# Optimization experiments

Hardware: AMD Instinct MI355X
Metric: run time of the kernel (lower is better)

The kernel has to match this reference:

```python
import jax, jax.numpy as jnp
import numpy as np
from jax import lax

# Model dims (mamba_ssm defaults: d_state=16, d_conv=4, expand=2, dt_rank=ceil(d_model/16))
V = 16384       # vocab_size
D = 1024        # embedding_dim / d_model
C_CLS = 128     # num_CLS_classes
D_INNER = 2 * D # expand * d_model = 2048
N = 16          # d_state
K = 4           # d_conv
DT_RANK = (D + 15) // 16  # 64
B, L = 4, 512


def setup_inputs() -> dict:
    key = jax.random.key(0)
    ks = jax.random.split(key, 12)
    s = 0.02
    tokens = jax.random.randint(ks[0], (B, L), 0, V, dtype=jnp.int64)
    embedding = jax.random.normal(ks[1], (V, D), jnp.float32) * s
    in_proj_w = jax.random.normal(ks[2], (2 * D_INNER, D), jnp.float32) * s
    conv_w = jax.random.normal(ks[3], (D_INNER, 1, K), jnp.float32) * 0.1
    conv_b = jnp.zeros((D_INNER,), jnp.float32)
    x_proj_w = jax.random.normal(ks[4], (DT_RANK + 2 * N, D_INNER), jnp.float32) * s
    dt_proj_w = jax.random.normal(ks[5], (D_INNER, DT_RANK), jnp.float32) * s
    dt_proj_b = jax.random.uniform(ks[6], (D_INNER,), jnp.float32, -4.0, -2.0)  # softplus -> small dt
    A_log = jnp.log(jnp.broadcast_to(jnp.arange(1, N + 1, dtype=jnp.float32), (D_INNER, N)))
    D_param = jnp.ones((D_INNER,), jnp.float32)
    out_proj_w = jax.random.normal(ks[7], (D, D_INNER), jnp.float32) * s
    recon_w = jax.random.normal(ks[8], (V, D), jnp.float32) * s
    cls_w = jax.random.normal(ks[9], (C_CLS, D), jnp.float32) * s
    return dict(tokens=tokens, embedding=embedding, in_proj_w=in_proj_w,
                conv_w=conv_w, conv_b=conv_b, x_proj_w=x_proj_w,
                dt_proj_w=dt_proj_w, dt_proj_b=dt_proj_b, A_log=A_log,
                D_param=D_param, out_proj_w=out_proj_w, recon_w=recon_w, cls_w=cls_w)


def _mamba(h, in_proj_w, conv_w, conv_b, x_proj_w, dt_proj_w, dt_proj_b, A_log, D_param, out_proj_w):
    # h: (B, L, D)
    xz = jnp.einsum('bld,ed->ble', h, in_proj_w)          # (B, L, 2*D_INNER)
    x, z = jnp.split(xz, 2, axis=-1)                      # each (B, L, D_INNER)
    # causal depthwise conv1d along L
    xt = jnp.swapaxes(x, 1, 2)                            # (B, D_INNER, L)
    xt = lax.conv_general_dilated(xt, conv_w, window_strides=(1,),
                                  padding=[(K - 1, 0)],
                                  feature_group_count=D_INNER,
                                  dimension_numbers=('NCH', 'OIH', 'NCH'))
    xt = xt + conv_b[None, :, None]
    x = jax.nn.silu(jnp.swapaxes(xt, 1, 2))               # (B, L, D_INNER)
    # input-dependent dt, B, C
    x_dbl = jnp.einsum('bld,ed->ble', x, x_proj_w)        # (B, L, DT_RANK+2N)
    dt, Bm, Cm = jnp.split(x_dbl, [DT_RANK, DT_RANK + N], axis=-1)
    delta = jax.nn.softplus(jnp.einsum('blr,dr->bld', dt, dt_proj_w) + dt_proj_b)  # (B,L,D_INNER)
    A = -jnp.exp(A_log)                                   # (D_INNER, N)
    dA = jnp.exp(delta[..., None] * A)                    # (B,L,D_INNER,N)
    dBx = delta[..., None] * Bm[:, :, None, :] * x[..., None]  # (B,L,D_INNER,N)
    # selective scan over time (sequential recurrence)
    dA_t = jnp.swapaxes(dA, 0, 1)                         # (L,B,D_INNER,N)
    dBx_t = jnp.swapaxes(dBx, 0, 1)
    C_t = jnp.swapaxes(Cm, 0, 1)                          # (L,B,N)
    def step(hc, inp):
        a, bx, c = inp
        hc = a * hc + bx                                  # (B,D_INNER,N)
        y = jnp.einsum('bdn,bn->bd', hc, c)
        return hc, y
    h0 = jnp.zeros((x.shape[0], D_INNER, N), x.dtype)
    _, ys = lax.scan(step, h0, (dA_t, dBx_t, C_t))
    y = jnp.swapaxes(ys, 0, 1) + x * D_param              # (B,L,D_INNER)
    y = y * jax.nn.silu(z)
    return jnp.einsum('ble,de->bld', y, out_proj_w)       # (B,L,D)


def reference(tokens, embedding, in_proj_w, conv_w, conv_b, x_proj_w,
              dt_proj_w, dt_proj_b, A_log, D_param, out_proj_w, recon_w, cls_w):
    h = embedding[tokens]                                 # (B,L,D)
    h = _mamba(h, in_proj_w, conv_w, conv_b, x_proj_w, dt_proj_w, dt_proj_b,
               A_log, D_param, out_proj_w)
    recon = jnp.einsum('bld,vd->blv', h, recon_w)         # (B,L,V)
    pooled = h.mean(axis=1)                               # mean CLS pooling assumption
    cls = jnp.einsum('bd,cd->bc', pooled, cls_w)          # (B,C_CLS)
    return (recon, cls)
```

## Files before the change

kernel.cpp:

```cpp
#include <hip/hip_runtime.h>
#include <hip/hip_bf16.h>
#include <stdint.h>

#define DIN    2048
#define MROWS  2048
#define LSEQ   512
#define NV     16384
#define DMODEL 1024
#define NC     8
#define CL     64

typedef __attribute__((ext_vector_type(8))) short bf16x8;
typedef __attribute__((ext_vector_type(4))) float f32x4;

__device__ __forceinline__ uint16_t f2bf(float f) {
  uint32_t u = __builtin_bit_cast(uint32_t, f);
  u += 0x7fffu + ((u >> 16) & 1u);
  return (uint16_t)(u >> 16);
}
__device__ __forceinline__ float bf2f(uint16_t u) {
  return __builtin_bit_cast(float, (uint32_t)u << 16);
}

__device__ __forceinline__ void gld_lds16(const uint16_t* g, uint16_t* l) {
  __builtin_amdgcn_global_load_lds(
      (const __attribute__((address_space(1))) void*)g,
      (__attribute__((address_space(3))) void*)l,
      16, 0, 0);
}

__global__ __launch_bounds__(512, 2) void gemm256_bf16_kernel(
    const uint16_t* __restrict__ A, const uint16_t* __restrict__ B,
    float* __restrict__ C, int M, int N, int K)
{
  __shared__ uint16_t lds[4 * 16384];
  const int tid = threadIdx.x;
  const int w   = tid >> 6;
  const int l   = tid & 63;

  const int nwg = gridDim.x;
  const int cpx = nwg >> 3;
  const int swz = (blockIdx.x & 7) * cpx + (blockIdx.x >> 3);
  const int nmy = M >> 8;
  const int bm  = (swz % nmy) << 8;
  const int bn  = (swz / nmy) << 8;

  const int fr = l & 15;
  const int fg = l >> 4;
  const int wr = w >> 2;
  const int wc = w & 3;

  const int srow = l >> 2;
  const int kof  = (((l & 3) ^ ((l >> 3) & 3)) << 3);
  const int ar0  = (w * 2 + 0) * 16 + srow;
  const int ar1  = (w * 2 + 1) * 16 + srow;
  const uint16_t* Ag0 = A + (size_t)(bm + ar0) * K + kof;
  const uint16_t* Ag1 = A + (size_t)(bm + ar1) * K + kof;
  const uint16_t* Bg0 = B + (size_t)(bn + ar0) * K + kof;
  const uint16_t* Bg1 = B + (size_t)(bn + ar1) * K + kof;
  const int lA0 = (w * 2 + 0) * 512;
  const int lA1 = (w * 2 + 1) * 512;
  const int lB0 = 8192 + (w * 2 + 0) * 512;
  const int lB1 = 8192 + (w * 2 + 1) * 512;

  const int axr  = ((fg ^ ((fr >> 1) & 3)) << 3);
  const int aoff = (wr * 128 + fr) * 32 + axr;
  const int boff = 8192 + (wc * 64 + fr) * 32 + axr;

  f32x4 acc[8][4] = {};
  const int NT = K >> 5;

  auto stage = [&](int t) {
    const int sb = (t & 3) << 14;
    const int k0 = t << 5;
    gld_lds16(Ag0 + k0, lds + sb + lA0);
    gld_lds16(Ag1 + k0, lds + sb + lA1);
    gld_lds16(Bg0 + k0, lds + sb + lB0);
    gld_lds16(Bg1 + k0, lds + sb + lB1);
  };
  auto compute_tile = [&](int sb) {
    bf16x8 af[8], bfr[4];
#pragma unroll
    for (int mi = 0; mi < 8; ++mi)
      af[mi] = *(const bf16x8*)(lds + sb + aoff + mi * 512);
#pragma unroll
    for (int ni = 0; ni < 4; ++ni)
      bfr[ni] = *(const bf16x8*)(lds + sb + boff + ni * 512);
    __builtin_amdgcn_s_setprio(1);
#pragma unroll
    for (int mi = 0; mi < 8; ++mi)
#pragma unroll
      for (int ni = 0; ni < 4; ++ni)
        acc[mi][ni] = __builtin_amdgcn_mfma_f32_16x16x32_bf16(af[mi], bfr[ni], acc[mi][ni], 0, 0, 0);
    __builtin_amdgcn_s_setprio(0);
  };

  stage(0); stage(1); stage(2);
  asm volatile("s_waitcnt vmcnt(8)" ::: "memory");
  __builtin_amdgcn_s_barrier();

  for (int t = 0; t < NT - 3; ++t) {
    stage(t + 3);
    compute_tile((t & 3) << 14);
    asm volatile("s_waitcnt vmcnt(8)" ::: "memory");
    __builtin_amdgcn_s_barrier();
  }
  compute_tile(((NT - 3) & 3) << 14);
  asm volatile("s_waitcnt vmcnt(4)" ::: "memory");
  __builtin_amdgcn_s_barrier();
  compute_tile(((NT - 2) & 3) << 14);
  asm volatile("s_waitcnt vmcnt(0)" ::: "memory");
  __builtin_amdgcn_s_barrier();
  compute_tile(((NT - 1) & 3) << 14);

#pragma unroll
  for (int mi = 0; mi < 8; ++mi) {
    const int r0 = bm + wr * 128 + mi * 16 + fg * 4;
#pragma unroll
    for (int ni = 0; ni < 4; ++ni) {
      const int c0 = bn + wc * 64 + ni * 16 + fr;
#pragma unroll
      for (int r = 0; r < 4; ++r)
        C[(size_t)(r0 + r) * N + c0] = acc[mi][ni][r];
    }
  }
}

__global__ __launch_bounds__(256) void gemm_bf16_kernel(
    const uint16_t* __restrict__ A, const uint16_t* __restrict__ B,
    float* __restrict__ Cf, uint16_t* __restrict__ Cbf,
    int M, int N, int K, int kchunk, const float* __restrict__ bias)
{
  __shared__ uint16_t As[128 * 32];
  __shared__ uint16_t Bs[128 * 32];
  const int tid  = threadIdx.x;
  const int wid  = tid >> 6;
  const int lane = tid & 63;
  const int bm = blockIdx.y * 128;
  const int bn = blockIdx.x * 128;
  const int k_beg = blockIdx.z * kchunk;
  float* Cout = Cf + (size_t)blockIdx.z * M * N;

  const int fr = lane & 15;
  const int fg = lane >> 4;
  const int wm = (wid >> 1) * 64;
  const int wn = (wid & 1) * 64;

  const int srow = wid * 32 + (lane >> 2);
  const int skof = (((lane & 3) ^ ((lane >> 2) & 3)) << 3);
  const uint16_t* Ag = A + (size_t)(bm + srow) * K + skof;
  const uint16_t* Bg = B + (size_t)(bn + srow) * K + skof;
  uint16_t* Al = As + wid * 1024;
  uint16_t* Bl = Bs + wid * 1024;

  const int cxr = ((fg ^ (fr & 3)) << 3);

  f32x4 acc[4][4] = {};

  for (int k0 = 0; k0 < kchunk; k0 += 32) {
    const int kk = k_beg + k0;
    gld_lds16(Ag + kk, Al);
    gld_lds16(Ag + (size_t)16 * K + kk, Al + 512);
    gld_lds16(Bg + kk, Bl);
    gld_lds16(Bg + (size_t)16 * K + kk, Bl + 512);
    asm volatile("s_waitcnt vmcnt(0)" ::: "memory");
    __syncthreads();
    bf16x8 af[4], bfr[4];
#pragma unroll
    for (int i = 0; i < 4; ++i)
      af[i] = *(const bf16x8*)(As + (wm + i * 16 + fr) * 32 + cxr);
#pragma unroll
    for (int j = 0; j < 4; ++j)
      bfr[j] = *(const bf16x8*)(Bs + (wn + j * 16 + fr) * 32 + cxr);
#pragma unroll
    for (int i = 0; i < 4; ++i)
#pragma unroll
      for (int j = 0; j < 4; ++j)
        acc[i][j] = __builtin_amdgcn_mfma_f32_16x16x32_bf16(af[i], bfr[j], acc[i][j], 0, 0, 0);
    __syncthreads();
  }

#pragma unroll
  for (int i = 0; i < 4; ++i) {
    const int r0 = bm + wm + i * 16 + fg * 4;
#pragma unroll
    for (int j = 0; j < 4; ++j) {
      const int c0 = bn + wn + j * 16 + fr;
      const float bv = bias ? bias[c0] : 0.f;
#pragma unroll
      for (int r = 0; r < 4; ++r) {
        float v = acc[i][j][r];
        if (bias) {
          const float u = v + bv;
          v = (u > 20.f) ? u : log1pf(__expf(u));
        }
        if (Cbf) Cbf[(size_t)(r0 + r) * N + c0] = f2bf(v);
        else     Cout[(size_t)(r0 + r) * N + c0] = v;
      }
    }
  }
}

__global__ __launch_bounds__(256) void mega_cvt_kernel(
    const int* __restrict__ tok, const float* __restrict__ emb,
    const float* __restrict__ wi, const float* __restrict__ wo,
    const float* __restrict__ wdt, const float* __restrict__ wx,
    uint16_t* __restrict__ hb, uint16_t* __restrict__ wib,
    uint16_t* __restrict__ wob, uint16_t* __restrict__ wdtb,
    uint16_t* __restrict__ wxb)
{
  const int bid = blockIdx.x;
  if (bid < 2048) {
    const int m = bid;
    const int t = tok[m];
    const float4 v = ((const float4*)(emb + (size_t)t * DMODEL))[threadIdx.x];
    ((ushort4*)(hb + (size_t)m * DMODEL))[threadIdx.x] =
        make_ushort4(f2bf(v.x), f2bf(v.y), f2bf(v.z), f2bf(v.w));
  } else if (bid < 6144) {
    const int i = (bid - 2048) * 256 + threadIdx.x;
    const float4 v = ((const float4*)wi)[i];
    ((ushort4*)wib)[i] = make_ushort4(f2bf(v.x), f2bf(v.y), f2bf(v.z), f2bf(v.w));
  } else if (bid < 8192) {
    const int i = (bid - 6144) * 256 + threadIdx.x;
    const float4 v = ((const float4*)wo)[i];
    ((ushort4*)wob)[i] = make_ushort4(f2bf(v.x), f2bf(v.y), f2bf(v.z), f2bf(v.w));
  } else if (bid < 8320) {
    const int i = (bid - 8192) * 256 + threadIdx.x;
    const float4 v = ((const float4*)wdt)[i];
    ((ushort4*)wdtb)[i] = make_ushort4(f2bf(v.x), f2bf(v.y), f2bf(v.z), f2bf(v.w));
  } else {
    const int i = (bid - 8320) * 256 + threadIdx.x;
    const int r = i >> 9, c = i & 511;
    ushort4 o = make_ushort4(0, 0, 0, 0);
    if (r < 96) {
      const float4 v = ((const float4*)wx)[(size_t)r * 512 + c];
      o = make_ushort4(f2bf(v.x), f2bf(v.y), f2bf(v.z), f2bf(v.w));
    }
    ((ushort4*)wxb)[i] = o;
  }
}

__global__ __launch_bounds__(256) void reduce8_dt_kernel(
    const float* __restrict__ in, float* __restrict__ xdbl, uint16_t* __restrict__ dtb) {
  const int i = blockIdx.x * 256 + threadIdx.x;
  float s = 0.f;
#pragma unroll
  for (int z = 0; z < 8; ++z) s += in[i + (size_t)z * 262144];
  xdbl[i] = s;
  const int c = i & 127;
  if (c < 64) dtb[(i >> 7) * 64 + c] = f2bf(s);
}

__global__ __launch_bounds__(256) void cvt_bf16_kernel(
    const float* __restrict__ in, uint16_t* __restrict__ out, int n4) {
  const int i = blockIdx.x * 256 + threadIdx.x;
  if (i >= n4) return;
  const float4 v = ((const float4*)in)[i];
  ((ushort4*)out)[i] = make_ushort4(f2bf(v.x), f2bf(v.y), f2bf(v.z), f2bf(v.w));
}

__global__ __launch_bounds__(256) void conv_silu_kernel(
    const uint16_t* __restrict__ xzb, const float* __restrict__ cw, const float* __restrict__ cb,
    uint16_t* __restrict__ xcb)
{
  const int idx = blockIdx.x * 256 + threadIdx.x;
  const int d4  = idx & 511;
  const int m   = idx >> 9;
  const int l   = m & (LSEQ - 1);
  const int d   = d4 << 2;
  const float4 cbv = *(const float4*)(cb + d);
  float a0 = cbv.x, a1 = cbv.y, a2 = cbv.z, a3 = cbv.w;
  const float4 w0 = *(const float4*)(cw + (d + 0) * 4);
  const float4 w1 = *(const float4*)(cw + (d + 1) * 4);
  const float4 w2 = *(const float4*)(cw + (d + 2) * 4);
  const float4 w3 = *(const float4*)(cw + (d + 3) * 4);
  const float wj0[4] = {w0.x, w0.y, w0.z, w0.w};
  const float wj1[4] = {w1.x, w1.y, w1.z, w1.w};
  const float wj2[4] = {w2.x, w2.y, w2.z, w2.w};
  const float wj3[4] = {w3.x, w3.y, w3.z, w3.w};
#pragma unroll
  for (int j = 0; j < 4; ++j) {
    const int lj = l - 3 + j;
    if (lj >= 0) {
      const ushort4 x = *(const ushort4*)(xzb + (size_t)(m - 3 + j) * 4096 + d);
      a0 += wj0[j] * bf2f(x.x);
      a1 += wj1[j] * bf2f(x.y);
      a2 += wj2[j] * bf2f(x.z);
      a3 += wj3[j] * bf2f(x.w);
    }
  }
  const float r0 = a0 / (1.f + __expf(-a0));
  const float r1 = a1 / (1.f + __expf(-a1));
  const float r2 = a2 / (1.f + __expf(-a2));
  const float r3 = a3 / (1.f + __expf(-a3));
  *(ushort4*)(xcb + (size_t)m * DIN + d) = make_ushort4(f2bf(r0), f2bf(r1), f2bf(r2), f2bf(r3));
}

__global__ __launch_bounds__(256) void scan_fused_kernel(
    const uint16_t* __restrict__ delta_bf, const uint16_t* __restrict__ xcb,
    const float* __restrict__ xdbl, const uint16_t* __restrict__ xzb,
    const float* __restrict__ A_log, const float* __restrict__ Dp,
    uint16_t* __restrict__ yb)
{
  __shared__ float Ps[NC][8][4][4];
  __shared__ float Qs[NC][8][4][4];
  __shared__ float Hs[NC][8][4][4];
  const int q = threadIdx.x & 3;
  const int d_idx = (threadIdx.x >> 2) & 7;
  const int c = threadIdx.x >> 5;
  const int d = blockIdx.x * 8 + d_idx;
  const int b = blockIdx.y;
  float Arow[4];
#pragma unroll
  for (int n = 0; n < 4; ++n)
    Arow[n] = -expf(A_log[d * 16 + q * 4 + n]);
  const int l0 = c * CL;

  float P[4] = {1.f, 1.f, 1.f, 1.f};
  float Q[4] = {0.f, 0.f, 0.f, 0.f};
#pragma unroll 4
  for (int li = 0; li < CL; ++li) {
    const int m = b * LSEQ + l0 + li;
    const float de = bf2f(delta_bf[(size_t)m * DIN + d]);
    const float xv = bf2f(xcb[(size_t)m * DIN + d]);
    const float dx = de * xv;
    const float4 Bv = *(const float4*)(xdbl + (size_t)m * 128 + 64 + q * 4);
    const float bv[4] = {Bv.x, Bv.y, Bv.z, Bv.w};
#pragma unroll
    for (int n = 0; n < 4; ++n) {
      const float a = __expf(de * Arow[n]);
      P[n] *= a;
      Q[n] = a * Q[n] + dx * bv[n];
    }
  }
#pragma unroll
  for (int n = 0; n < 4; ++n) {
    Ps[c][d_idx][q][n] = P[n];
    Qs[c][d_idx][q][n] = Q[n];
  }
  __syncthreads();

  if (threadIdx.x < 32) {
    float h[4] = {0.f, 0.f, 0.f, 0.f};
#pragma unroll
    for (int cc = 0; cc < NC; ++cc) {
#pragma unroll
      for (int n = 0; n < 4; ++n) {
        Hs[cc][d_idx][q][n] = h[n];
        h[n] = Ps[cc][d_idx][q][n] * h[n] + Qs[cc][d_idx][q][n];
      }
    }
  }
  __syncthreads();

  float h[4];
#pragma unroll
  for (int n = 0; n < 4; ++n) h[n] = Hs[c][d_idx][q][n];
  const float dpd = Dp[d];
#pragma unroll 2
  for (int li = 0; li < CL; ++li) {
    const int m = b * LSEQ + l0 + li;
    const float de = bf2f(delta_bf[(size_t)m * DIN + d]);
    const float xv = bf2f(xcb[(size_t)m * DIN + d]);
    const float dx = de * xv;
    const float4 Bv = *(const float4*)(xdbl + (size_t)m * 128 + 64 + q * 4);
    const float4 Cv = *(const float4*)(xdbl + (size_t)m * 128 + 80 + q * 4);
    const float bv[4] = {Bv.x, Bv.y, Bv.z, Bv.w};
    const float cv[4] = {Cv.x, Cv.y, Cv.z, Cv.w};
    float yp = 0.f;
#pragma unroll
    for (int n = 0; n < 4; ++n) {
      const float a = __expf(de * Arow[n]);
      h[n] = a * h[n] + dx * bv[n];
      yp += h[n] * cv[n];
    }
    yp += __shfl_xor(yp, 1);
    yp += __shfl_xor(yp, 2);
    if (q == 0) {
      const float z = bf2f(xzb[(size_t)m * 4096 + 2048 + d]);
      const float sil = z / (1.f + __expf(-z));
      yb[(size_t)m * DIN + d] = f2bf((yp + xv * dpd) * sil);
    }
  }
}

__global__ __launch_bounds__(256) void pool1_kernel(
    const uint16_t* __restrict__ h2b, float* __restrict__ part) {
  const int b = blockIdx.x >> 4, s = blockIdx.x & 15;
  const int c = threadIdx.x * 4;
  const uint16_t* base = h2b + ((size_t)(b * LSEQ + s * 32)) * DMODEL + c;
  float a0 = 0, a1 = 0, a2 = 0, a3 = 0;
  for (int l = 0; l < 32; ++l) {
    const ushort4 v = *(const ushort4*)(base + (size_t)l * DMODEL);
    a0 += bf2f(v.x); a1 += bf2f(v.y); a2 += bf2f(v.z); a3 += bf2f(v.w);
  }
  *(float4*)(part + (size_t)blockIdx.x * DMODEL + c) = make_float4(a0, a1, a2, a3);
}

__global__ __launch_bounds__(256) void pool2_cls_kernel(
    const float* __restrict__ part, const float* __restrict__ w, float* __restrict__ out) {
  __shared__ float pl[DMODEL];
  const int b = blockIdx.x, t = threadIdx.x;
  float4 s = make_float4(0, 0, 0, 0);
  for (int k = 0; k < 16; ++k) {
    const float4 v = *(const float4*)(part + ((size_t)(b * 16 + k)) * DMODEL + t * 4);
    s.x += v.x; s.y += v.y; s.z += v.z; s.w += v.w;
  }
  const float inv = 1.f / (float)LSEQ;
  pl[t * 4 + 0] = s.x * inv; pl[t * 4 + 1] = s.y * inv;
  pl[t * 4 + 2] = s.z * inv; pl[t * 4 + 3] = s.w * inv;
  __syncthreads();
  if (t < 128) {
    const float* wr = w + (size_t)t * DMODEL;
    float acc = 0.f;
    for (int k = 0; k < DMODEL; ++k) acc += pl[k] * wr[k];
    out[b * 128 + t] = acc;
  }
}

extern "C" void kernel_launch(void* const* d_in, const int* in_sizes, int n_in,
                              void* d_out, int out_size, void* d_ws, size_t ws_size,
                              hipStream_t stream) {
  const int*   tokens    = (const int*)d_in[0];
  const float* embedding = (const float*)d_in[1];
  const float* in_proj_w = (const float*)d_in[2];
  const float* conv_w    = (const float*)d_in[3];
  const float* conv_b    = (const float*)d_in[4];
  const float* x_proj_w  = (const float*)d_in[5];
  const float* dt_proj_w = (const float*)d_in[6];
  const float* dt_proj_b = (const float*)d_in[7];
  const float* A_log     = (const float*)d_in[8];
  const float* D_param   = (const float*)d_in[9];
  const float* out_prj_w = (const float*)d_in[10];
  const float* recon_w   = (const float*)d_in[11];
  const float* cls_w     = (const float*)d_in[12];

  char* ws = (char*)d_ws;
  const size_t MB = 1024 * 1024;
  uint16_t* h_bf   = (uint16_t*)(ws + 0);
  uint16_t* w_in   = (uint16_t*)(ws + 4 * MB);
  uint16_t* xz_bf  = (uint16_t*)(ws + 12 * MB);
  uint16_t* xc_b   = (uint16_t*)(ws + 28 * MB);
  uint16_t* wx_bf  = (uint16_t*)(ws + 36 * MB);
  uint16_t* dt_bf  = (uint16_t*)(ws + 36 * MB + 512 * 1024);
  uint16_t* wdt_bf = (uint16_t*)(ws + 36 * MB + 768 * 1024);
  float*    xdbl   = (float*)(ws + 37 * MB);
  uint16_t* delt_b = (uint16_t*)(ws + 38 * MB);
  float*    kscr   = (float*)(ws + 46 * MB);
  uint16_t* y_bf   = (uint16_t*)(ws + 54 * MB);
  uint16_t* h2_bf  = (uint16_t*)(ws + 62 * MB);
  uint16_t* wout_bf= (uint16_t*)(ws + 66 * MB);
  float*    part   = (float*)(ws + 70 * MB);
  uint16_t* wrec_bf= (uint16_t*)(ws + 71 * MB);

  const int RECON = MROWS * NV;

  mega_cvt_kernel<<<dim3(8576), dim3(256), 0, stream>>>(
      tokens, embedding, in_proj_w, out_prj_w, dt_proj_w, x_proj_w,
      h_bf, w_in, wout_bf, wdt_bf, wx_bf);
  gemm_bf16_kernel<<<dim3(32, 16, 1), dim3(256), 0, stream>>>(h_bf, w_in, nullptr, xz_bf, MROWS, 4096, 1024, 1024, nullptr);
  conv_silu_kernel<<<dim3(4096), dim3(256), 0, stream>>>(xz_bf, conv_w, conv_b, xc_b);
  gemm_bf16_kernel<<<dim3(1, 16, 8), dim3(256), 0, stream>>>(xc_b, wx_bf, kscr, nullptr, MROWS, 128, 2048, 256, nullptr);
  reduce8_dt_kernel<<<dim3(1024), dim3(256), 0, stream>>>(kscr, xdbl, dt_bf);
  gemm_bf16_kernel<<<dim3(16, 16, 1), dim3(256), 0, stream>>>(dt_bf, wdt_bf, nullptr, delt_b, MROWS, DIN, 64, 64, dt_proj_b);
  scan_fused_kernel<<<dim3(DIN / 8, 4), dim3(256), 0, stream>>>(delt_b, xc_b, xdbl, xz_bf, A_log, D_param, y_bf);
  gemm_bf16_kernel<<<dim3(8, 16, 1), dim3(256), 0, stream>>>(y_bf, wout_bf, nullptr, h2_bf, MROWS, 1024, 2048, 2048, nullptr);
  cvt_bf16_kernel<<<dim3(16384), dim3(256), 0, stream>>>(recon_w, wrec_bf, NV * 1024 / 4);
  gemm256_bf16_kernel<<<dim3(512), dim3(512), 0, stream>>>(h2_bf, wrec_bf, (float*)d_out, MROWS, NV, 1024);
  pool1_kernel<<<dim3(64), dim3(256), 0, stream>>>(h2_bf, part);
  pool2_cls_kernel<<<dim3(4), dim3(256), 0, stream>>>(part, cls_w, (float*)d_out + RECON);
}
```

Before: 402.5 us.

## Split selective scan into partial, chunk-carry, and final kernels with per-thread channels

Replaces the single fused scan kernel, which used four threads per channel and in-block chunk carry propagation, with three kernels. In the new scheme each thread owns one channel with all 16 states, chunk summaries P/Q are written to global memory, and a separate kernel computes chunk initial states. This removes the shuffle reduction, the shared-memory sync and redundant B/C loads per thread. In exchange it adds two launches and global round-trips for P, Q and H, and cuts total thread count fourfold, which lowers occupancy.

```diff
diff --git a/kernel.cpp b/kernel.cpp
--- a/kernel.cpp
+++ b/kernel.cpp
@@ -296,91 +296,107 @@
   *(ushort4*)(xcb + (size_t)m * DIN + d) = make_ushort4(f2bf(r0), f2bf(r1), f2bf(r2), f2bf(r3));
 }
 
-__global__ __launch_bounds__(256) void scan_fused_kernel(
+__global__ __launch_bounds__(256) void scan_partial_kernel(
     const uint16_t* __restrict__ delta_bf, const uint16_t* __restrict__ xcb,
-    const float* __restrict__ xdbl, const uint16_t* __restrict__ xzb,
-    const float* __restrict__ A_log, const float* __restrict__ Dp,
-    uint16_t* __restrict__ yb)
-{
-  __shared__ float Ps[NC][8][4][4];
-  __shared__ float Qs[NC][8][4][4];
-  __shared__ float Hs[NC][8][4][4];
-  const int q = threadIdx.x & 3;
-  const int d_idx = (threadIdx.x >> 2) & 7;
-  const int c = threadIdx.x >> 5;
-  const int d = blockIdx.x * 8 + d_idx;
-  const int b = blockIdx.y;
-  float Arow[4];
-#pragma unroll
-  for (int n = 0; n < 4; ++n)
-    Arow[n] = -expf(A_log[d * 16 + q * 4 + n]);
+    const float* __restrict__ xdbl, const float* __restrict__ A_log,
+    float* __restrict__ Pb, float* __restrict__ Qb)
+{
+  const int c = blockIdx.x;
+  const int d = blockIdx.y * 256 + threadIdx.x;
+  const int b = blockIdx.z;
+  float Arow[16], P[16], Q[16];
+#pragma unroll
+  for (int n = 0; n < 16; ++n) {
+    Arow[n] = -expf(A_log[d * 16 + n]);
+    P[n] = 1.f; Q[n] = 0.f;
+  }
   const int l0 = c * CL;
-
-  float P[4] = {1.f, 1.f, 1.f, 1.f};
-  float Q[4] = {0.f, 0.f, 0.f, 0.f};
-#pragma unroll 4
   for (int li = 0; li < CL; ++li) {
     const int m = b * LSEQ + l0 + li;
     const float de = bf2f(delta_bf[(size_t)m * DIN + d]);
     const float xv = bf2f(xcb[(size_t)m * DIN + d]);
     const float dx = de * xv;
-    const float4 Bv = *(const float4*)(xdbl + (size_t)m * 128 + 64 + q * 4);
-    const float bv[4] = {Bv.x, Bv.y, Bv.z, Bv.w};
-#pragma unroll
-    for (int n = 0; n < 4; ++n) {
+    const float4 B0 = *(const float4*)(xdbl + (size_t)m * 128 + 64);
+    const float4 B1 = *(const float4*)(xdbl + (size_t)m * 128 + 68);
+    const float4 B2 = *(const float4*)(xdbl + (size_t)m * 128 + 72);
+    const float4 B3 = *(const float4*)(xdbl + (size_t)m * 128 + 76);
+    const float bv[16] = {B0.x, B0.y, B0.z, B0.w, B1.x, B1.y, B1.z, B1.w,
+                          B2.x, B2.y, B2.z, B2.w, B3.x, B3.y, B3.z, B3.w};
+#pragma unroll
+    for (int n = 0; n < 16; ++n) {
       const float a = __expf(de * Arow[n]);
       P[n] *= a;
       Q[n] = a * Q[n] + dx * bv[n];
     }
   }
-#pragma unroll
-  for (int n = 0; n < 4; ++n) {
-    Ps[c][d_idx][q][n] = P[n];
-    Qs[c][d_idx][q][n] = Q[n];
-  }
-  __syncthreads();
-
-  if (threadIdx.x < 32) {
-    float h[4] = {0.f, 0.f, 0.f, 0.f};
-#pragma unroll
-    for (int cc = 0; cc < NC; ++cc) {
-#pragma unroll
-      for (int n = 0; n < 4; ++n) {
-        Hs[cc][d_idx][q][n] = h[n];
-        h[n] = Ps[cc][d_idx][q][n] * h[n] + Qs[cc][d_idx][q][n];
-      }
-    }
-  }
-  __syncthreads();
-
-  float h[4];
-#pragma unroll
-  for (int n = 0; n < 4; ++n) h[n] = Hs[c][d_idx][q][n];
+  const size_t base = ((size_t)(b * NC + c) * 16) * DIN + d;
+#pragma unroll
+  for (int n = 0; n < 16; ++n) {
+    Pb[base + (size_t)n * DIN] = P[n];
+    Qb[base + (size_t)n * DIN] = Q[n];
+  }
+}
+
+__global__ __launch_bounds__(256) void scan_bounds_kernel(
+    const float* __restrict__ Pb, const float* __restrict__ Qb, float* __restrict__ Hi)
+{
+  const int i = blockIdx.x * 256 + threadIdx.x;
+  const int b = i >> 15;
+  const int r = i & 32767;
+  float h = 0.f;
+#pragma unroll
+  for (int c = 0; c < NC; ++c) {
+    const size_t o = ((size_t)(b * NC + c) << 15) + r;
+    Hi[o] = h;
+    h = Pb[o] * h + Qb[o];
+  }
+}
+
+__global__ __launch_bounds__(256) void scan_final_kernel(
+    const uint16_t* __restrict__ delta_bf, const uint16_t* __restrict__ xcb,
+    const float* __restrict__ xdbl, const uint16_t* __restrict__ xzb,
+    const float* __restrict__ A_log, const float* __restrict__ Dp,
+    const float* __restrict__ Hi, uint16_t* __restrict__ yb)
+{
+  const int c = blockIdx.x;
+  const int d = blockIdx.y * 256 + threadIdx.x;
+  const int b = blockIdx.z;
+  float Arow[16], h[16];
+  const size_t base = ((size_t)(b * NC + c) * 16) * DIN + d;
+#pragma unroll
+  for (int n = 0; n < 16; ++n) {
+    Arow[n] = -expf(A_log[d * 16 + n]);
+    h[n] = Hi[base + (size_t)n * DIN];
+  }
   const float dpd = Dp[d];
-#pragma unroll 2
+  const int l0 = c * CL;
   for (int li = 0; li < CL; ++li) {
     const int m = b * LSEQ + l0 + li;
     const float de = bf2f(delta_bf[(size_t)m * DIN + d]);
     const float xv = bf2f(xcb[(size_t)m * DIN + d]);
     const float dx = de * xv;
-    const float4 Bv = *(const float4*)(xdbl + (size_t)m * 128 + 64 + q * 4);
-    const float4 Cv = *(const float4*)(xdbl + (size_t)m * 128 + 80 + q * 4);
-    const float bv[4] = {Bv.x, Bv.y, Bv.z, Bv.w};
-    const float cv[4] = {Cv.x, Cv.y, Cv.z, Cv.w};
+    const float4 B0 = *(const float4*)(xdbl + (size_t)m * 128 + 64);
+    const float4 B1 = *(const float4*)(xdbl + (size_t)m * 128 + 68);
+    const float4 B2 = *(const float4*)(xdbl + (size_t)m * 128 + 72);
+    const float4 B3 = *(const float4*)(xdbl + (size_t)m * 128 + 76);
+    const float4 C0 = *(const float4*)(xdbl + (size_t)m * 128 + 80);
+    const float4 C1 = *(const float4*)(xdbl + (size_t)m * 128 + 84);
+    const float4 C2 = *(const float4*)(xdbl + (size_t)m * 128 + 88);
+    const float4 C3 = *(const float4*)(xdbl + (size_t)m * 128 + 92);
+    const float bv[16] = {B0.x, B0.y, B0.z, B0.w, B1.x, B1.y, B1.z, B1.w,
+                          B2.x, B2.y, B2.z, B2.w, B3.x, B3.y, B3.z, B3.w};
+    const float cv[16] = {C0.x, C0.y, C0.z, C0.w, C1.x, C1.y, C1.z, C1.w,
+                          C2.x, C2.y, C2.z, C2.w, C3.x, C3.y, C3.z, C3.w};
     float yp = 0.f;
 #pragma unroll
-    for (int n = 0; n < 4; ++n) {
+    for (int n = 0; n < 16; ++n) {
       const float a = __expf(de * Arow[n]);
       h[n] = a * h[n] + dx * bv[n];
       yp += h[n] * cv[n];
     }
-    yp += __shfl_xor(yp, 1);
-    yp += __shfl_xor(yp, 2);
-    if (q == 0) {
-      const float z = bf2f(xzb[(size_t)m * 4096 + 2048 + d]);
-      const float sil = z / (1.f + __expf(-z));
-      yb[(size_t)m * DIN + d] = f2bf((yp + xv * dpd) * sil);
-    }
+    const float z = bf2f(xzb[(size_t)m * 4096 + 2048 + d]);
+    const float sil = z / (1.f + __expf(-z));
+    yb[(size_t)m * DIN + d] = f2bf((yp + xv * dpd) * sil);
   }
 }
 
@@ -452,6 +468,9 @@
   uint16_t* wout_bf= (uint16_t*)(ws + 66 * MB);
   float*    part   = (float*)(ws + 70 * MB);
   uint16_t* wrec_bf= (uint16_t*)(ws + 71 * MB);
+  float*    Pbuf   = (float*)(ws + 46 * MB);
+  float*    Qbuf   = (float*)(ws + 50 * MB);
+  float*    Hinit  = (float*)(ws + 0);
 
   const int RECON = MROWS * NV;
 
@@ -463,7 +482,9 @@
   gemm_bf16_kernel<<<dim3(1, 16, 8), dim3(256), 0, stream>>>(xc_b, wx_bf, kscr, nullptr, MROWS, 128, 2048, 256, nullptr);
   reduce8_dt_kernel<<<dim3(1024), dim3(256), 0, stream>>>(kscr, xdbl, dt_bf);
   gemm_bf16_kernel<<<dim3(16, 16, 1), dim3(256), 0, stream>>>(dt_bf, wdt_bf, nullptr, delt_b, MROWS, DIN, 64, 64, dt_proj_b);
-  scan_fused_kernel<<<dim3(DIN / 8, 4), dim3(256), 0, stream>>>(delt_b, xc_b, xdbl, xz_bf, A_log, D_param, y_bf);
+  scan_partial_kernel<<<dim3(NC, 8, 4), dim3(256), 0, stream>>>(delt_b, xc_b, xdbl, A_log, Pbuf, Qbuf);
+  scan_bounds_kernel<<<dim3(512), dim3(256), 0, stream>>>(Pbuf, Qbuf, Hinit);
+  scan_final_kernel<<<dim3(NC, 8, 4), dim3(256), 0, stream>>>(delt_b, xc_b, xdbl, xz_bf, A_log, D_param, Hinit, y_bf);
   gemm_bf16_kernel<<<dim3(8, 16, 1), dim3(256), 0, stream>>>(y_bf, wout_bf, nullptr, h2_bf, MROWS, 1024, 2048, 2048, nullptr);
   cvt_bf16_kernel<<<dim3(16384), dim3(256), 0, stream>>>(recon_w, wrec_bf, NV * 1024 / 4);
   gemm256_bf16_kernel<<<dim3(512), dim3(512), 0, stream>>>(h2_bf, wrec_bf, (float*)d_out, MROWS, NV, 1024);
```

Measured after the change: 371.9 us. 1.08x faster.
